# Optimization experiments

Measured on AMD Instinct MI355X. Metric: run time of the kernel, lower is better.

The kernel has to match this reference:

```python
import jax, jax.numpy as jnp
import numpy as np

ALPHA = 0.2  # leaky-relu negative slope AND the residual scale self.alpha

def setup_inputs() -> dict:
    key = jax.random.key(0)
    k1, k2, k3 = jax.random.split(key, 3)
    B, N, C_in, C_out = 8, 2048, 128, 128
    text = jax.random.normal(k1, (B, N, C_in), dtype=jnp.float32)
    adj = jnp.ones((B, N, N), dtype=jnp.float32)  # unused by the layer's forward
    W = jax.random.normal(k2, (C_in, C_out), dtype=jnp.float32) * (1.414 / np.sqrt(C_in + C_out))
    a = jax.random.normal(k3, (2 * C_out, 1), dtype=jnp.float32) * (1.414 / np.sqrt(2 * C_out + 1))
    return {"text": text, "adj": adj, "W": W, "a": a}

def reference(text, adj, W, a):
    # text: [B,N,C_in]; adj is unused (faithful to the source forward).
    h = jnp.einsum('bnc,cf->bnf', text, W)                  # [B,N,F]
    F_out = W.shape[1]
    a1 = a[:F_out, 0]                                       # score contribution of node i
    a2 = a[F_out:, 0]                                       # score contribution of node j
    s1 = jnp.einsum('bnf,f->bn', h, a1)                     # [B,N]
    s2 = jnp.einsum('bnf,f->bn', h, a2)                     # [B,N]
    # leakyrelu(cat(h_i,h_j) @ a) == leakyrelu(s1_i + s2_j): avoids O(N^2*2F) concat
    e = jax.nn.leaky_relu(s1[:, :, None] + s2[:, None, :], negative_slope=ALPHA)  # [B,N,N]
    attention = jax.nn.softmax(e, axis=2)                   # dropout is a no-op in eval mode
    h_prime = jnp.einsum('bij,bjf->bif', attention, h)      # [B,N,F]
    return jax.nn.elu(h_prime + ALPHA * h)
```

## Files before the change

### kernel.cpp

```cpp
#include <hip/hip_runtime.h>
#include <hip/hip_bf16.h>
#include <math.h>

#define LRELU_ALPHA 0.2f

constexpr int B_ = 8;
constexpr int N_ = 2048;
constexpr int M_ = B_ * N_;
constexpr int SEG = 32;
constexpr int NSEG = N_ / SEG;

__global__ __launch_bounds__(256) void k_gemm(const float* __restrict__ text,
                                              const float* __restrict__ W,
                                              const float* __restrict__ a,
                                              float* __restrict__ h,
                                              float* __restrict__ s1,
                                              float* __restrict__ s2,
                                              float* __restrict__ eN0,
                                              float* __restrict__ eP0,
                                              int* __restrict__ bcnt) {
    __shared__ __align__(16) float As[64 * 132];
    __shared__ __align__(16) float Ws[128 * 128];

    const int tid = threadIdx.x;
    const int blk = blockIdx.x;

    if (blk == 0)
        for (int t = tid; t < B_ * NSEG; t += 256) bcnt[t] = 0;

    const int r0  = blk * 64;
    const int cx  = tid & 15;
    const int ry  = tid >> 4;
    const int c0  = cx * 4;
    const int c1  = 64 + cx * 4;
    const int rr0 = ry * 4;

    for (int idx = tid; idx < 64 * 32; idx += 256) {
        int r = idx >> 5, k4 = (idx & 31) * 4;
        *(float4*)&As[r * 132 + k4] =
            *(const float4*)&text[(size_t)(r0 + r) * 128 + k4];
    }
    for (int idx = tid; idx < 128 * 32; idx += 256) {
        int k = idx >> 5, f4 = (idx & 31) * 4;
        *(float4*)&Ws[k * 128 + f4] = *(const float4*)&W[(size_t)k * 128 + f4];
    }
    __syncthreads();

    float acc[4][8];
#pragma unroll
    for (int i = 0; i < 4; ++i)
#pragma unroll
        for (int j = 0; j < 8; ++j) acc[i][j] = 0.f;

#pragma unroll 2
    for (int k0 = 0; k0 < 128; k0 += 4) {
        float4 av[4];
#pragma unroll
        for (int i = 0; i < 4; ++i)
            av[i] = *(const float4*)&As[(rr0 + i) * 132 + k0];
#pragma unroll
        for (int kk = 0; kk < 4; ++kk) {
            float4 w0 = *(const float4*)&Ws[(k0 + kk) * 128 + c0];
            float4 w1 = *(const float4*)&Ws[(k0 + kk) * 128 + c1];
#pragma unroll
            for (int i = 0; i < 4; ++i) {
                const float avv = (kk == 0) ? av[i].x : (kk == 1) ? av[i].y
                                : (kk == 2) ? av[i].z : av[i].w;
                acc[i][0] += avv * w0.x; acc[i][1] += avv * w0.y;
                acc[i][2] += avv * w0.z; acc[i][3] += avv * w0.w;
                acc[i][4] += avv * w1.x; acc[i][5] += avv * w1.y;
                acc[i][6] += avv * w1.z; acc[i][7] += avv * w1.w;
            }
        }
    }

    float4 a1lo = *(const float4*)&a[c0];
    float4 a1hi = *(const float4*)&a[c1];
    float4 a2lo = *(const float4*)&a[128 + c0];
    float4 a2hi = *(const float4*)&a[128 + c1];

#pragma unroll
    for (int i = 0; i < 4; ++i) {
        const int row = r0 + rr0 + i;
        float4 o0 = {acc[i][0], acc[i][1], acc[i][2], acc[i][3]};
        float4 o1 = {acc[i][4], acc[i][5], acc[i][6], acc[i][7]};
        *(float4*)&h[(size_t)row * 128 + c0] = o0;
        *(float4*)&h[(size_t)row * 128 + c1] = o1;

        float p1 = o0.x*a1lo.x + o0.y*a1lo.y + o0.z*a1lo.z + o0.w*a1lo.w
                 + o1.x*a1hi.x + o1.y*a1hi.y + o1.z*a1hi.z + o1.w*a1hi.w;
        float p2 = o0.x*a2lo.x + o0.y*a2lo.y + o0.z*a2lo.z + o0.w*a2lo.w
                 + o1.x*a2hi.x + o1.y*a2hi.y + o1.z*a2hi.z + o1.w*a2hi.w;
#pragma unroll
        for (int off = 8; off >= 1; off >>= 1) {
            p1 += __shfl_xor(p1, off);
            p2 += __shfl_xor(p2, off);
        }
        if (cx == 0) {
            s1[row] = p1;
            s2[row] = p2;
            eN0[row] = expf(LRELU_ALPHA * p2);
            eP0[row] = expf(p2);
        }
    }
}

__global__ __launch_bounds__(512) void k_rank(const float* __restrict__ s2,
                                              const float* __restrict__ eN0,
                                              const float* __restrict__ eP0,
                                              const float* __restrict__ s1,
                                              int* __restrict__ perm,
                                              float* __restrict__ eNs,
                                              float* __restrict__ ePs,
                                              float* __restrict__ ZN,
                                              float* __restrict__ ZP,
                                              int* __restrict__ bcnt,
                                              int* __restrict__ bucket) {
    __shared__ float ls2[2048], leN[2048], leP[2048];
    __shared__ int   redc[512], redm[512];
    __shared__ float redn[512], redp[512];

    const int b  = blockIdx.x >> 5;
    const int eb = blockIdx.x & 31;
    const int tid = threadIdx.x;
    const int e = tid & 63;
    const int c = tid >> 6;

    {
        const float4* g2 = (const float4*)(s2  + b * 2048);
        const float4* gn = (const float4*)(eN0 + b * 2048);
        const float4* gp = (const float4*)(eP0 + b * 2048);
        ((float4*)ls2)[tid] = g2[tid];
        ((float4*)leN)[tid] = gn[tid];
        ((float4*)leP)[tid] = gp[tid];
    }
    __syncthreads();

    const int i  = eb * 64 + e;
    const int gi = b * 2048 + i;
    const float myS2 = ls2[i];
    const float thr  = -s1[gi];

    int cnt = 0, mr = 0;
    float sn = 0.f, sp = 0.f;
    const int j0 = c * 256;
#pragma unroll 4
    for (int j = j0; j < j0 + 256; j += 4) {
        float4 v  = *(const float4*)&ls2[j];
        float4 en = *(const float4*)&leN[j];
        float4 ep = *(const float4*)&leP[j];
#define PROC(vv, ee, pp, jj)                                             \
        { bool le = (vv) <= thr;                                         \
          cnt += le ? 1 : 0;                                             \
          sn  += le ? (ee) : 0.f;                                        \
          sp  += le ? 0.f : (pp);                                        \
          mr  += ((vv) < myS2 || ((vv) == myS2 && (jj) < i)) ? 1 : 0; }
        PROC(v.x, en.x, ep.x, j + 0)
        PROC(v.y, en.y, ep.y, j + 1)
        PROC(v.z, en.z, ep.z, j + 2)
        PROC(v.w, en.w, ep.w, j + 3)
#undef PROC
    }
    redc[tid] = cnt; redm[tid] = mr; redn[tid] = sn; redp[tid] = sp;
    __syncthreads();
    if (c == 0) {
        int tc = 0, tm = 0; float tn = 0.f, tp = 0.f;
#pragma unroll
        for (int cc = 0; cc < 8; ++cc) {
            tc += redc[cc * 64 + e];
            tm += redm[cc * 64 + e];
            tn += redn[cc * 64 + e];
            tp += redp[cc * 64 + e];
        }
        perm[b * 2048 + tm] = i;
        eNs [b * 2048 + tm] = leN[i];
        ePs [b * 2048 + tm] = leP[i];
        ZN[gi] = tn;
        ZP[gi] = tp;
        const int seg = min(tc >> 5, NSEG - 1);
        const int pos = atomicAdd(&bcnt[b * NSEG + seg], 1);
        if (pos < 2048)
            bucket[(b * NSEG + seg) * 2048 + pos] = i | (tc << 11);
    }
}

__global__ __launch_bounds__(128) void k_segsum(const float* __restrict__ h,
                                                const int* __restrict__ perm,
                                                const float* __restrict__ eNs,
                                                const float* __restrict__ ePs,
                                                float* __restrict__ segN,
                                                float* __restrict__ segP) {
    const int blk = blockIdx.x;
    const int b = blk >> 6, s = blk & 63;
    const int f = threadIdx.x;
    const int rr0 = b * 2048 + s * SEG;

    int pm[SEG];
#pragma unroll
    for (int r = 0; r < SEG; ++r) pm[r] = perm[rr0 + r];
    float hv[SEG];
#pragma unroll
    for (int r = 0; r < SEG; ++r)
        hv[r] = h[(size_t)(b * 2048 + pm[r]) * 128 + f];

    float an = 0.f, ap = 0.f;
#pragma unroll
    for (int r = 0; r < SEG; ++r) {
        an += eNs[rr0 + r] * hv[r];
        ap += ePs[rr0 + r] * hv[r];
    }
    segN[blk * 128 + f] = an;
    segP[blk * 128 + f] = ap;
}

__global__ __launch_bounds__(128) void k_scanout(
    const float* __restrict__ h, const int* __restrict__ perm,
    const float* __restrict__ eNs, const float* __restrict__ ePs,
    const float* __restrict__ s1,
    const float* __restrict__ ZN, const float* __restrict__ ZP,
    const float* __restrict__ segN, const float* __restrict__ segP,
    const int* __restrict__ bcnt, const int* __restrict__ bucket,
    float* __restrict__ out) {

    __shared__ float anL[(SEG + 1) * 128];
    __shared__ float apL[(SEG + 1) * 128];

    const int blk = blockIdx.x;
    const int b = blk >> 6, s = blk & 63;
    const int f = threadIdx.x;

    float bn = 0.f, bp = 0.f;
    for (int ss = 0; ss < s; ++ss)        bn += segN[(b * NSEG + ss) * 128 + f];
    for (int ss = s + 1; ss < NSEG; ++ss) bp += segP[(b * NSEG + ss) * 128 + f];

    const int rr0 = b * 2048 + s * SEG;
    int pm[SEG];
#pragma unroll
    for (int r = 0; r < SEG; ++r) pm[r] = perm[rr0 + r];
    float hv[SEG];
#pragma unroll
    for (int r = 0; r < SEG; ++r)
        hv[r] = h[(size_t)(b * 2048 + pm[r]) * 128 + f];

    float an = bn;
#pragma unroll
    for (int r = 0; r < SEG; ++r) {
        anL[r * 128 + f] = an;
        an += eNs[rr0 + r] * hv[r];
    }
    anL[SEG * 128 + f] = an;

    float ap = bp;
    apL[SEG * 128 + f] = ap;
#pragma unroll
    for (int r = SEG - 1; r >= 0; --r) {
        ap += ePs[rr0 + r] * hv[r];
        apL[r * 128 + f] = ap;
    }
    __syncthreads();

    const int m = min(bcnt[b * NSEG + s], 2048);
    for (int t = 0; t < m; ++t) {
        const int packed = bucket[(b * NSEG + s) * 2048 + t];
        const int il = packed & 2047;
        const int tc = packed >> 11;
        const int gi = b * 2048 + il;
        const int pl = tc - s * SEG;
        const float s1v = s1[gi];
        const float E1 = expf(s1v);
        const float E2 = expf(LRELU_ALPHA * s1v);
        const float Z  = E1 * ZP[gi] + E2 * ZN[gi];
        const float hp = (E1 * apL[pl * 128 + f] + E2 * anL[pl * 128 + f]) / Z;
        const float x  = hp + LRELU_ALPHA * h[(size_t)gi * 128 + f];
        out[(size_t)gi * 128 + f] = (x > 0.f) ? x : expm1f(x);
    }
}

extern "C" void kernel_launch(void* const* d_in, const int* in_sizes, int n_in,
                              void* d_out, int out_size, void* d_ws, size_t ws_size,
                              hipStream_t stream) {
    const float* text = (const float*)d_in[0];
    const float* W = (const float*)d_in[2];
    const float* a = (const float*)d_in[3];
    float* out = (float*)d_out;

    float* p = (float*)d_ws;
    float* h    = p; p += (size_t)M_ * 128;
    float* s1   = p; p += M_;
    float* s2   = p; p += M_;
    float* eN0  = p; p += M_;
    float* eP0  = p; p += M_;
    int*   perm = (int*)p; p += M_;
    float* eNs  = p; p += M_;
    float* ePs  = p; p += M_;
    float* ZN   = p; p += M_;
    float* ZP   = p; p += M_;
    float* segN = p; p += B_ * NSEG * 128;
    float* segP = p; p += B_ * NSEG * 128;
    int*   bcnt = (int*)p; p += B_ * NSEG;
    int*   bucket = (int*)p; p += (size_t)B_ * NSEG * 2048;

    hipLaunchKernelGGL(k_gemm,   dim3(M_ / 64),   dim3(256), 0, stream,
                       text, W, a, h, s1, s2, eN0, eP0, bcnt);
    hipLaunchKernelGGL(k_rank,   dim3(B_ * 32),   dim3(512), 0, stream,
                       s2, eN0, eP0, s1, perm, eNs, ePs, ZN, ZP, bcnt, bucket);
    hipLaunchKernelGGL(k_segsum, dim3(B_ * NSEG), dim3(128), 0, stream,
                       h, perm, eNs, ePs, segN, segP);
    hipLaunchKernelGGL(k_scanout, dim3(B_ * NSEG), dim3(128), 0, stream,
                       h, perm, eNs, ePs, s1, ZN, ZP, segN, segP,
                       bcnt, bucket, out);
}
```

Before: 244.5 us.

## Fuse segment sums into rank kernel via atomics and split scanout across two halves

Removes the separate segment-sum kernel. The rank kernel now scatters each row's weighted h contributions into per-segment accumulators with atomicAdd, and the GEMM kernel zeroes those accumulators first. The scan/output kernel doubles its threads so one half builds the negative prefix and the other the positive suffix, and the two halves share the bucket loop. This saves a launch and one gather of h, at the cost of many float atomics and nondeterministic summation order.

Result: slower. 253.8 us (+3.8%).

```diff
diff --git a/kernel.cpp b/kernel.cpp
--- a/kernel.cpp
+++ b/kernel.cpp
@@ -18,6 +18,8 @@
                                               float* __restrict__ s2,
                                               float* __restrict__ eN0,
                                               float* __restrict__ eP0,
+                                              float* __restrict__ segN,
+                                              float* __restrict__ segP,
                                               int* __restrict__ bcnt) {
     __shared__ __align__(16) float As[64 * 132];
     __shared__ __align__(16) float Ws[128 * 128];
@@ -25,8 +27,13 @@
     const int tid = threadIdx.x;
     const int blk = blockIdx.x;
 
-    if (blk == 0)
-        for (int t = tid; t < B_ * NSEG; t += 256) bcnt[t] = 0;
+    {
+        const int g = blk * 256 + tid;
+        segN[g] = 0.f;
+        segP[g] = 0.f;
+        if (blk == 0)
+            for (int t = tid; t < B_ * NSEG; t += 256) bcnt[t] = 0;
+    }
 
     const int r0  = blk * 64;
     const int cx  = tid & 15;
@@ -109,16 +116,20 @@
                                               const float* __restrict__ eN0,
                                               const float* __restrict__ eP0,
                                               const float* __restrict__ s1,
+                                              const float* __restrict__ h,
                                               int* __restrict__ perm,
                                               float* __restrict__ eNs,
                                               float* __restrict__ ePs,
                                               float* __restrict__ ZN,
                                               float* __restrict__ ZP,
+                                              float* __restrict__ segN,
+                                              float* __restrict__ segP,
                                               int* __restrict__ bcnt,
                                               int* __restrict__ bucket) {
     __shared__ float ls2[2048], leN[2048], leP[2048];
     __shared__ int   redc[512], redm[512];
     __shared__ float redn[512], redp[512];
+    __shared__ int   tmL[64];
 
     const int b  = blockIdx.x >> 5;
     const int eb = blockIdx.x & 31;
@@ -177,43 +188,30 @@
         ePs [b * 2048 + tm] = leP[i];
         ZN[gi] = tn;
         ZP[gi] = tp;
+        tmL[e] = tm;
         const int seg = min(tc >> 5, NSEG - 1);
         const int pos = atomicAdd(&bcnt[b * NSEG + seg], 1);
         if (pos < 2048)
             bucket[(b * NSEG + seg) * 2048 + pos] = i | (tc << 11);
     }
+    __syncthreads();
+
+    {
+        const int f  = tid & 127;
+        const int q  = tid >> 7;
+#pragma unroll 4
+        for (int it = 0; it < 16; ++it) {
+            const int rl = it * 4 + q;
+            const int ii = eb * 64 + rl;
+            const int sg = tmL[rl] >> 5;
+            const float hvv = h[(size_t)(b * 2048 + ii) * 128 + f];
+            atomicAdd(&segN[(b * NSEG + sg) * 128 + f], leN[ii] * hvv);
+            atomicAdd(&segP[(b * NSEG + sg) * 128 + f], leP[ii] * hvv);
+        }
+    }
 }
 
-__global__ __launch_bounds__(128) void k_segsum(const float* __restrict__ h,
-                                                const int* __restrict__ perm,
-                                                const float* __restrict__ eNs,
-                                                const float* __restrict__ ePs,
-                                                float* __restrict__ segN,
-                                                float* __restrict__ segP) {
-    const int blk = blockIdx.x;
-    const int b = blk >> 6, s = blk & 63;
-    const int f = threadIdx.x;
-    const int rr0 = b * 2048 + s * SEG;
-
-    int pm[SEG];
-#pragma unroll
-    for (int r = 0; r < SEG; ++r) pm[r] = perm[rr0 + r];
-    float hv[SEG];
-#pragma unroll
-    for (int r = 0; r < SEG; ++r)
-        hv[r] = h[(size_t)(b * 2048 + pm[r]) * 128 + f];
-
-    float an = 0.f, ap = 0.f;
-#pragma unroll
-    for (int r = 0; r < SEG; ++r) {
-        an += eNs[rr0 + r] * hv[r];
-        ap += ePs[rr0 + r] * hv[r];
-    }
-    segN[blk * 128 + f] = an;
-    segP[blk * 128 + f] = ap;
-}
-
-__global__ __launch_bounds__(128) void k_scanout(
+__global__ __launch_bounds__(256) void k_scanout(
     const float* __restrict__ h, const int* __restrict__ perm,
     const float* __restrict__ eNs, const float* __restrict__ ePs,
     const float* __restrict__ s1,
@@ -227,52 +225,62 @@
 
     const int blk = blockIdx.x;
     const int b = blk >> 6, s = blk & 63;
-    const int f = threadIdx.x;
-
-    float bn = 0.f, bp = 0.f;
-    for (int ss = 0; ss < s; ++ss)        bn += segN[(b * NSEG + ss) * 128 + f];
-    for (int ss = s + 1; ss < NSEG; ++ss) bp += segP[(b * NSEG + ss) * 128 + f];
+    const int tid = threadIdx.x;
+    const int f  = tid & 127;
+    const int hf = tid >> 7;
 
     const int rr0 = b * 2048 + s * SEG;
+    const float* es = hf ? ePs : eNs;
     int pm[SEG];
 #pragma unroll
     for (int r = 0; r < SEG; ++r) pm[r] = perm[rr0 + r];
+    float ev[SEG];
+#pragma unroll
+    for (int r = 0; r < SEG; ++r) ev[r] = es[rr0 + r];
     float hv[SEG];
 #pragma unroll
     for (int r = 0; r < SEG; ++r)
         hv[r] = h[(size_t)(b * 2048 + pm[r]) * 128 + f];
 
-    float an = bn;
-#pragma unroll
-    for (int r = 0; r < SEG; ++r) {
-        anL[r * 128 + f] = an;
-        an += eNs[rr0 + r] * hv[r];
-    }
-    anL[SEG * 128 + f] = an;
-
-    float ap = bp;
-    apL[SEG * 128 + f] = ap;
-#pragma unroll
-    for (int r = SEG - 1; r >= 0; --r) {
-        ap += ePs[rr0 + r] * hv[r];
-        apL[r * 128 + f] = ap;
+    if (hf == 0) {
+        float an = 0.f;
+        for (int ss = 0; ss < s; ++ss) an += segN[(b * NSEG + ss) * 128 + f];
+#pragma unroll
+        for (int r = 0; r < SEG; ++r) {
+            anL[r * 128 + f] = an;
+            an += ev[r] * hv[r];
+        }
+        anL[SEG * 128 + f] = an;
+    } else {
+        float ap = 0.f;
+        for (int ss = s + 1; ss < NSEG; ++ss) ap += segP[(b * NSEG + ss) * 128 + f];
+        apL[SEG * 128 + f] = ap;
+#pragma unroll
+        for (int r = SEG - 1; r >= 0; --r) {
+            ap += ev[r] * hv[r];
+            apL[r * 128 + f] = ap;
+        }
     }
     __syncthreads();
 
     const int m = min(bcnt[b * NSEG + s], 2048);
-    for (int t = 0; t < m; ++t) {
-        const int packed = bucket[(b * NSEG + s) * 2048 + t];
-        const int il = packed & 2047;
-        const int tc = packed >> 11;
-        const int gi = b * 2048 + il;
-        const int pl = tc - s * SEG;
-        const float s1v = s1[gi];
-        const float E1 = expf(s1v);
-        const float E2 = expf(LRELU_ALPHA * s1v);
-        const float Z  = E1 * ZP[gi] + E2 * ZN[gi];
-        const float hp = (E1 * apL[pl * 128 + f] + E2 * anL[pl * 128 + f]) / Z;
-        const float x  = hp + LRELU_ALPHA * h[(size_t)gi * 128 + f];
-        out[(size_t)gi * 128 + f] = (x > 0.f) ? x : expm1f(x);
+    for (int t0 = 0; t0 < m; t0 += 2) {
+        const int t = t0 + hf;
+        if (t < m) {
+            const int packed = bucket[(b * NSEG + s) * 2048 + t];
+            const int il = packed & 2047;
+            const int tc = packed >> 11;
+            const int gi = b * 2048 + il;
+            const int pl = tc - s * SEG;
+            const float s1v = s1[gi];
+            const float E1 = expf(s1v);
+            const float E2 = expf(LRELU_ALPHA * s1v);
+            const float Z  = E1 * ZP[gi] + E2 * ZN[gi];
+            const float hp = (E1 * apL[pl * 128 + f]
+                            + E2 * anL[pl * 128 + f]) / Z;
+            const float x  = hp + LRELU_ALPHA * h[(size_t)gi * 128 + f];
+            out[(size_t)gi * 128 + f] = (x > 0.f) ? x : expm1f(x);
+        }
     }
 }
 
@@ -301,12 +309,11 @@
     int*   bucket = (int*)p; p += (size_t)B_ * NSEG * 2048;
 
     hipLaunchKernelGGL(k_gemm,   dim3(M_ / 64),   dim3(256), 0, stream,
-                       text, W, a, h, s1, s2, eN0, eP0, bcnt);
+                       text, W, a, h, s1, s2, eN0, eP0, segN, segP, bcnt);
     hipLaunchKernelGGL(k_rank,   dim3(B_ * 32),   dim3(512), 0, stream,
-                       s2, eN0, eP0, s1, perm, eNs, ePs, ZN, ZP, bcnt, bucket);
-    hipLaunchKernelGGL(k_segsum, dim3(B_ * NSEG), dim3(128), 0, stream,
-                       h, perm, eNs, ePs, segN, segP);
-    hipLaunchKernelGGL(k_scanout, dim3(B_ * NSEG), dim3(128), 0, stream,
+                       s2, eN0, eP0, s1, h, perm, eNs, ePs, ZN, ZP,
+                       segN, segP, bcnt, bucket);
+    hipLaunchKernelGGL(k_scanout, dim3(B_ * NSEG), dim3(256), 0, stream,
                        h, perm, eNs, ePs, s1, ZN, ZP, segN, segP,
                        bcnt, bucket, out);
 }
```
